# Kernel optimization log

Measured on AMD Instinct MI355X. Metric: run time of the kernel, lower is better.

Reference implementation:

```python
import jax, jax.numpy as jnp
import numpy as np

D_STATE = 64
HEADDIM = 64
D_CONV = 4
EPS = 1e-5


def _layernorm(x, w, b):
    m = jnp.mean(x, -1, keepdims=True)
    v = jnp.mean((x - m) ** 2, -1, keepdims=True)
    return (x - m) * jax.lax.rsqrt(v + EPS) * w + b


def _mamba2(x, W_in, conv_w, conv_b, dt_bias, A_log, Dh, rms_w, W_out):
    # Mamba2 (SSD) forward: in_proj -> causal depthwise conv + silu -> selective scan
    # -> gated RMSNorm -> out_proj.  ngroups=1, headdim=64, d_state=64.
    Bb, L, _ = x.shape
    d_inner = rms_w.shape[0]
    H = dt_bias.shape[0]
    P = d_inner // H
    conv_dim = d_inner + 2 * D_STATE
    zxbcdt = x @ W_in                                   # [B,L,2*d_inner+2*N+H]
    z = zxbcdt[..., :d_inner]
    xBC = zxbcdt[..., d_inner:d_inner + conv_dim]
    dt = zxbcdt[..., d_inner + conv_dim:]               # [B,L,H]
    # causal depthwise conv1d (kernel D_CONV) + bias + silu
    xpad = jnp.pad(xBC, ((0, 0), (D_CONV - 1, 0), (0, 0)))
    xBC = sum(conv_w[k] * xpad[:, k:k + L] for k in range(D_CONV)) + conv_b
    xBC = jax.nn.silu(xBC)
    xh = xBC[..., :d_inner].reshape(Bb, L, H, P)        # [B,L,H,P]
    Bm = xBC[..., d_inner:d_inner + D_STATE]            # [B,L,N]
    Cm = xBC[..., d_inner + D_STATE:]                   # [B,L,N]
    dt = jax.nn.softplus(dt + dt_bias)                  # [B,L,H]
    A = -jnp.exp(A_log)                                 # [H]
    da = jnp.exp(dt * A)                                # [B,L,H] discrete decay
    dtx = dt[..., None] * xh                            # [B,L,H,P]

    def step(h, inp):
        da_t, dtx_t, B_t, C_t = inp
        h = da_t[:, :, None, None] * h + jnp.einsum('bhp,bn->bhpn', dtx_t, B_t)
        y_t = jnp.einsum('bhpn,bn->bhp', h, C_t)
        return h, y_t

    h0 = jnp.zeros((Bb, H, P, D_STATE), x.dtype)
    _, y = jax.lax.scan(step, h0, (da.transpose(1, 0, 2), dtx.transpose(1, 0, 2, 3),
                                   Bm.transpose(1, 0, 2), Cm.transpose(1, 0, 2)))
    y = y.transpose(1, 0, 2, 3) + Dh[None, None, :, None] * xh   # skip term
    y = y.reshape(Bb, L, d_inner)
    # gated RMSNorm (norm_before_gate=False): rmsnorm(y * silu(z)) * weight
    y = y * jax.nn.silu(z)
    y = y * jax.lax.rsqrt(jnp.mean(y * y, -1, keepdims=True) + EPS) * rms_w
    return y @ W_out


def _mamba_params(key, d_model, pre):
    d_inner = 2 * d_model
    H = d_inner // HEADDIM
    conv_dim = d_inner + 2 * D_STATE
    d_in = 2 * d_inner + 2 * D_STATE + H
    k = jax.random.split(key, 5)
    return {
        pre + '_W_in': jax.random.normal(k[0], (d_model, d_in), jnp.float32) * (d_model ** -0.5),
        pre + '_conv_w': jax.random.normal(k[1], (D_CONV, conv_dim), jnp.float32) * 0.2,
        pre + '_conv_b': jnp.zeros((conv_dim,), jnp.float32),
        pre + '_dt_bias': jnp.log(jnp.expm1(jax.random.uniform(k[2], (H,), jnp.float32, 0.001, 0.1))),
        pre + '_A_log': jnp.log(jax.random.uniform(k[3], (H,), jnp.float32, 1.0, 16.0)),
        pre + '_D': jnp.ones((H,), jnp.float32),
        pre + '_rms_w': jnp.ones((d_inner,), jnp.float32),
        pre + '_W_out': jax.random.normal(k[4], (d_inner, d_model), jnp.float32) * (d_inner ** -0.5),
    }


def setup_inputs() -> dict:
    key = jax.random.key(0)
    ks = jax.random.split(key, 3)
    B, L, C = 8, 1024, 128
    inp = {'x': jax.random.normal(ks[0], (B, L, C), jnp.float32)}
    inp['ln_spa_w'] = jnp.ones((C,), jnp.float32)
    inp['ln_spa_b'] = jnp.zeros((C,), jnp.float32)
    inp['ln_spe_w'] = jnp.ones((L,), jnp.float32)
    inp['ln_spe_b'] = jnp.zeros((L,), jnp.float32)
    inp.update(_mamba_params(ks[1], C, 'spa'))
    inp.update(_mamba_params(ks[2], L, 'spe'))
    return inp


def reference(x, ln_spa_w, ln_spa_b, ln_spe_w, ln_spe_b,
              spa_W_in, spa_conv_w, spa_conv_b, spa_dt_bias, spa_A_log, spa_D, spa_rms_w, spa_W_out,
              spe_W_in, spe_conv_w, spe_conv_b, spe_dt_bias, spe_A_log, spe_D, spe_rms_w, spe_W_out):
    # SSD_Block.forward (drop_path=0 -> identity)
    x_spa = _layernorm(x, ln_spa_w, ln_spa_b)
    x_spa = _mamba2(x_spa, spa_W_in, spa_conv_w, spa_conv_b, spa_dt_bias,
                    spa_A_log, spa_D, spa_rms_w, spa_W_out) + x
    x_spe = x_spa.transpose(0, 2, 1)                      # [B,C,L]
    x_spe = _layernorm(x_spe, ln_spe_w, ln_spe_b)
    x_spe = _mamba2(x_spe, spe_W_in, spe_conv_w, spe_conv_b, spe_dt_bias,
                    spe_A_log, spe_D, spe_rms_w, spe_W_out)
    return x_spe.transpose(0, 2, 1) + x_spa
```

## Files before the change

kernel.cpp:

```cpp
#include <hip/hip_runtime.h>
#include <hip/hip_bf16.h>

#define EPSV 1e-5f

typedef __attribute__((ext_vector_type(8))) short short8v;
typedef __attribute__((ext_vector_type(4))) float f32x4;

__device__ inline unsigned short f2bf(float f) {
  __hip_bfloat16 h = __float2bfloat16(f);
  return *reinterpret_cast<unsigned short*>(&h);
}

__device__ inline float bf2f(unsigned short u) {
  return __uint_as_float(((unsigned int)u) << 16);
}

__device__ inline float siluf(float x) { return x / (1.f + expf(-x)); }

__device__ inline void gload_lds16(const void* g, void* l) {
  __builtin_amdgcn_global_load_lds(
      (const __attribute__((address_space(1))) void*)g,
      (__attribute__((address_space(3))) void*)l, 16, 0, 0);
}

__device__ inline float wave_prefix_incl(float v, int lane) {
  #pragma unroll
  for (int o = 1; o < 64; o <<= 1) {
    float u = __shfl_up(v, o);
    if (lane >= o) v += u;
  }
  return v;
}

__device__ inline void wtconv_tile(const float* __restrict__ W,
                                   unsigned short* __restrict__ Wt,
                                   int K, int N, int bx, int by) {
  __shared__ float tile[64][65];
  int n0 = bx * 64, k0 = by * 64;
  int tid = threadIdx.x;
  int r = tid >> 4, c4 = (tid & 15) * 4;
  #pragma unroll
  for (int i = 0; i < 4; i++) {
    int kk = r + i * 16;
    float4 v = make_float4(0.f, 0.f, 0.f, 0.f);
    if (n0 + c4 < N) v = *reinterpret_cast<const float4*>(&W[(long)(k0 + kk) * N + n0 + c4]);
    tile[kk][c4] = v.x; tile[kk][c4 + 1] = v.y; tile[kk][c4 + 2] = v.z; tile[kk][c4 + 3] = v.w;
  }
  __syncthreads();
  #pragma unroll
  for (int i = 0; i < 4; i++) {
    int nl = r + i * 16;
    if (n0 + nl < N) {
      ushort4 o;
      o.x = f2bf(tile[c4 + 0][nl]);
      o.y = f2bf(tile[c4 + 1][nl]);
      o.z = f2bf(tile[c4 + 2][nl]);
      o.w = f2bf(tile[c4 + 3][nl]);
      *reinterpret_cast<ushort4*>(&Wt[(long)(n0 + nl) * K + k0 + c4]) = o;
    }
  }
}

__global__ __launch_bounds__(256) void ln_wt_fused(const float* __restrict__ x,
                                                   const float* __restrict__ w,
                                                   const float* __restrict__ bb,
                                                   unsigned short* __restrict__ outA,
                                                   const float* __restrict__ W0,
                                                   unsigned short* __restrict__ T0,
                                                   const float* __restrict__ W1,
                                                   unsigned short* __restrict__ T1,
                                                   const float* __restrict__ W2,
                                                   unsigned short* __restrict__ T2,
                                                   const float* __restrict__ W3,
                                                   unsigned short* __restrict__ T3) {
  int id = blockIdx.x;
  if (id < 4096) {
    int tid = threadIdx.x;
    __shared__ float lds[4];
    long row = (long)id * 2 + (tid >> 7);
    int lane = tid & 127;
    int base = (tid >> 7) << 1;
    float v = x[row * 128 + lane];
    float s = v;
    #pragma unroll
    for (int o = 32; o; o >>= 1) s += __shfl_xor(s, o);
    if ((tid & 63) == 0) lds[tid >> 6] = s;
    __syncthreads();
    float m = (lds[base] + lds[base + 1]) * (1.f / 128.f);
    float d = v - m;
    float q = d * d;
    #pragma unroll
    for (int o = 32; o; o >>= 1) q += __shfl_xor(q, o);
    __syncthreads();
    if ((tid & 63) == 0) lds[tid >> 6] = q;
    __syncthreads();
    float inv = rsqrtf((lds[base] + lds[base + 1]) * (1.f / 128.f) + EPSV);
    outA[row * 128 + lane] = f2bf(d * inv * w[lane] + bb[lane]);
  } else {
    id -= 4096;
    if (id < 22)        { int r = id;        wtconv_tile(W0, T0, 128,  644,  r % 11, r / 11); }
    else if (id < 30)   { int r = id - 22;   wtconv_tile(W1, T1, 256,  128,  r % 2,  r / 2); }
    else if (id < 1102) { int r = id - 30;   wtconv_tile(W2, T2, 1024, 4256, r % 67, r / 67); }
    else                { int r = id - 1102; wtconv_tile(W3, T3, 2048, 1024, r % 16, r / 16); }
  }
}

__global__ __launch_bounds__(256) void spe_normT(const float* __restrict__ xspa,
                                                 const float* __restrict__ part2,
                                                 const float* __restrict__ w,
                                                 const float* __restrict__ bb,
                                                 unsigned short* __restrict__ out) {
  __shared__ float tile[128][65];
  int c0 = blockIdx.x * 64, l0 = blockIdx.y * 128, b = blockIdx.z;
  int tid = threadIdx.x;
  int rr = tid >> 4, c4 = (tid & 15) * 4;
  #pragma unroll
  for (int p = 0; p < 8; p++) {
    int l = rr + p * 16;
    f32x4 v = *reinterpret_cast<const f32x4*>(
        &xspa[((long)b * 1024 + l0 + l) * 128 + c0 + c4]);
    tile[l][c4] = v[0]; tile[l][c4 + 1] = v[1];
    tile[l][c4 + 2] = v[2]; tile[l][c4 + 3] = v[3];
  }
  __syncthreads();
  int ch = tid >> 2, lq = tid & 3;
  int gc = c0 + ch;
  int bx = gc >> 6, cl = gc & 63;
  float ssum = 0.f, qsum = 0.f;
  #pragma unroll
  for (int sub = 0; sub < 16; sub++) {
    int by = b * 16 + sub;
    float2 pq = *reinterpret_cast<const float2*>(&part2[(((by * 2 + bx) * 64) + cl) * 2]);
    ssum += pq.x; qsum += pq.y;
  }
  float mm = ssum * (1.f / 1024.f);
  float rstd = rsqrtf(qsum * (1.f / 1024.f) - mm * mm + EPSV);
  #pragma unroll
  for (int j = 0; j < 8; j++) {
    int qidx = lq + j * 4;
    int l = qidx * 4;
    float4 wv = *reinterpret_cast<const float4*>(&w[l0 + l]);
    float4 bv = *reinterpret_cast<const float4*>(&bb[l0 + l]);
    ushort4 o;
    o.x = f2bf((tile[l + 0][ch] - mm) * rstd * wv.x + bv.x);
    o.y = f2bf((tile[l + 1][ch] - mm) * rstd * wv.y + bv.y);
    o.z = f2bf((tile[l + 2][ch] - mm) * rstd * wv.z + bv.z);
    o.w = f2bf((tile[l + 3][ch] - mm) * rstd * wv.w + bv.w);
    *reinterpret_cast<ushort4*>(&out[((long)b * 128 + c0 + ch) * 1024 + l0 + l]) = o;
  }
}

__global__ __launch_bounds__(256) void gemm128_split(const unsigned short* __restrict__ A,
                                                     const unsigned short* __restrict__ Bt,
                                                     unsigned short* __restrict__ zout,
                                                     unsigned short* __restrict__ o2,
                                                     float* __restrict__ o3,
                                                     int M, int N, int K,
                                                     int c1, int c2) {
  __shared__ unsigned short As[2][128 * 32];
  __shared__ unsigned short Bs[2][128 * 32];
  int tid = threadIdx.x;
  int lane = tid & 63, w = tid >> 6;
  int wr = (w >> 1) * 64, wc = (w & 1) * 64;
  int ln15 = lane & 15, kg = lane >> 4;
  int rowBase = blockIdx.y * 128, colBase = blockIdx.x * 128;
  int srow = w * 32 + (lane >> 2);
  int scol = (lane & 3) * 8;
  f32x4 acc[4][4] = {};
  auto stage = [&](int buf, int k0) {
    gload_lds16(&A[(long)(rowBase + srow) * K + k0 + scol], &As[buf][(w * 32) * 32]);
    gload_lds16(&A[(long)(rowBase + srow + 16) * K + k0 + scol], &As[buf][(w * 32 + 16) * 32]);
    gload_lds16(&Bt[(long)(colBase + srow) * K + k0 + scol], &Bs[buf][(w * 32) * 32]);
    gload_lds16(&Bt[(long)(colBase + srow + 16) * K + k0 + scol], &Bs[buf][(w * 32 + 16) * 32]);
  };
  stage(0, 0);
  __syncthreads();
  int cur = 0;
  for (int k0 = 0; k0 < K; k0 += 32) {
    if (k0 + 32 < K) stage(cur ^ 1, k0 + 32);
    short8v af[4], bfr[4];
    #pragma unroll
    for (int mt = 0; mt < 4; mt++)
      af[mt] = *reinterpret_cast<const short8v*>(&As[cur][(wr + mt * 16 + ln15) * 32 + kg * 8]);
    #pragma unroll
    for (int nt = 0; nt < 4; nt++)
      bfr[nt] = *reinterpret_cast<const short8v*>(&Bs[cur][(wc + nt * 16 + ln15) * 32 + kg * 8]);
    #pragma unroll
    for (int mt = 0; mt < 4; mt++)
      #pragma unroll
      for (int nt = 0; nt < 4; nt++)
        acc[mt][nt] = __builtin_amdgcn_mfma_f32_16x16x32_bf16(af[mt], bfr[nt], acc[mt][nt], 0, 0, 0);
    __syncthreads();
    cur ^= 1;
  }
  #pragma unroll
  for (int mt = 0; mt < 4; mt++)
    #pragma unroll
    for (int nt = 0; nt < 4; nt++)
      #pragma unroll
      for (int q = 0; q < 4; q++) {
        int r = rowBase + wr + mt * 16 + kg * 4 + q;
        int c = colBase + wc + nt * 16 + ln15;
        if (c < N) {
          float v = acc[mt][nt][q];
          if (c < c1) zout[(long)r * c1 + c] = f2bf(v);
          else if (c < c2) o2[(long)r * (c2 - c1) + (c - c1)] = f2bf(v);
          else o3[(long)r * (N - c2) + (c - c2)] = v;
        }
      }
}

__global__ __launch_bounds__(256) void gemm128x64_t(const unsigned short* __restrict__ A,
                                                    const unsigned short* __restrict__ Bt,
                                                    const float* __restrict__ R,
                                                    float* __restrict__ out,
                                                    int M, int N, int K) {
  __shared__ unsigned short As[2][128 * 32];
  __shared__ unsigned short Bs[2][64 * 32];
  int tid = threadIdx.x;
  int lane = tid & 63, w = tid >> 6;
  int wr = w * 32;
  int ln15 = lane & 15, kg = lane >> 4;
  int rowBase = blockIdx.y * 128, colBase = blockIdx.x * 64;
  int arow = w * 32 + (lane >> 2);
  int brow = w * 16 + (lane >> 2);
  int scol = (lane & 3) * 8;
  f32x4 acc[2][4] = {};
  auto stage = [&](int buf, int k0) {
    gload_lds16(&A[(long)(rowBase + arow) * K + k0 + scol], &As[buf][(w * 32) * 32]);
    gload_lds16(&A[(long)(rowBase + arow + 16) * K + k0 + scol], &As[buf][(w * 32 + 16) * 32]);
    gload_lds16(&Bt[(long)(colBase + brow) * K + k0 + scol], &Bs[buf][(w * 16) * 32]);
  };
  stage(0, 0);
  __syncthreads();
  int cur = 0;
  for (int k0 = 0; k0 < K; k0 += 32) {
    if (k0 + 32 < K) stage(cur ^ 1, k0 + 32);
    short8v af[2], bfr[4];
    #pragma unroll
    for (int mt = 0; mt < 2; mt++)
      af[mt] = *reinterpret_cast<const short8v*>(&As[cur][(wr + mt * 16 + ln15) * 32 + kg * 8]);
    #pragma unroll
    for (int nt = 0; nt < 4; nt++)
      bfr[nt] = *reinterpret_cast<const short8v*>(&Bs[cur][(nt * 16 + ln15) * 32 + kg * 8]);
    #pragma unroll
    for (int mt = 0; mt < 2; mt++)
      #pragma unroll
      for (int nt = 0; nt < 4; nt++)
        acc[mt][nt] = __builtin_amdgcn_mfma_f32_16x16x32_bf16(af[mt], bfr[nt], acc[mt][nt], 0, 0, 0);
    __syncthreads();
    cur ^= 1;
  }
  #pragma unroll
  for (int mt = 0; mt < 2; mt++)
    #pragma unroll
    for (int nt = 0; nt < 4; nt++)
      #pragma unroll
      for (int q = 0; q < 4; q++) {
        int r = rowBase + wr + mt * 16 + kg * 4 + q;
        int c = colBase + nt * 16 + ln15;
        int bb = r >> 7, ch = r & 127;
        out[(long)bb * 131072 + (long)c * 128 + ch] =
            acc[mt][nt][q] + R[((long)bb * 1024 + c) * 128 + ch];
      }
}

__global__ __launch_bounds__(256) void gemm_mfma1(const unsigned short* __restrict__ A,
                                                  const unsigned short* __restrict__ Bt,
                                                  const float* __restrict__ R,
                                                  float* __restrict__ out,
                                                  float* __restrict__ part2,
                                                  int M, int N, int K) {
  __shared__ unsigned short As[2][64 * 32];
  __shared__ unsigned short Bs[2][64 * 32];
  int tid = threadIdx.x;
  int lane = tid & 63, w = tid >> 6;
  int wr = (w >> 1) * 32, wc = (w & 1) * 32;
  int ln15 = lane & 15, kg = lane >> 4;
  int rowBase = blockIdx.y * 64, colBase = blockIdx.x * 64;
  int srow = w * 16 + (lane >> 2);
  int scol = (lane & 3) * 8;
  f32x4 acc[2][2] = {};
  auto stage = [&](int buf, int k0) {
    gload_lds16(&A[(long)(rowBase + srow) * K + k0 + scol], &As[buf][(w * 16) * 32]);
    gload_lds16(&Bt[(long)(colBase + srow) * K + k0 + scol], &Bs[buf][(w * 16) * 32]);
  };
  stage(0, 0);
  __syncthreads();
  int cur = 0;
  for (int k0 = 0; k0 < K; k0 += 32) {
    if (k0 + 32 < K) stage(cur ^ 1, k0 + 32);
    short8v af[2], bfr[2];
    #pragma unroll
    for (int mt = 0; mt < 2; mt++)
      af[mt] = *reinterpret_cast<const short8v*>(&As[cur][(wr + mt * 16 + ln15) * 32 + kg * 8]);
    #pragma unroll
    for (int nt = 0; nt < 2; nt++)
      bfr[nt] = *reinterpret_cast<const short8v*>(&Bs[cur][(wc + nt * 16 + ln15) * 32 + kg * 8]);
    #pragma unroll
    for (int mt = 0; mt < 2; mt++)
      #pragma unroll
      for (int nt = 0; nt < 2; nt++)
        acc[mt][nt] = __builtin_amdgcn_mfma_f32_16x16x32_bf16(af[mt], bfr[nt], acc[mt][nt], 0, 0, 0);
    __syncthreads();
    cur ^= 1;
  }
  float sC[2] = {0.f, 0.f}, qC[2] = {0.f, 0.f};
  #pragma unroll
  for (int mt = 0; mt < 2; mt++)
    #pragma unroll
    for (int nt = 0; nt < 2; nt++)
      #pragma unroll
      for (int q = 0; q < 4; q++) {
        int r = rowBase + wr + mt * 16 + kg * 4 + q;
        int c = colBase + wc + nt * 16 + ln15;
        float v = acc[mt][nt][q] + R[(long)r * N + c];
        out[(long)r * N + c] = v;
        sC[nt] += v;
        qC[nt] += v * v;
      }
  __shared__ float redS[4][32], redQ[4][32];
  #pragma unroll
  for (int nt = 0; nt < 2; nt++) {
    sC[nt] += __shfl_xor(sC[nt], 16);
    sC[nt] += __shfl_xor(sC[nt], 32);
    qC[nt] += __shfl_xor(qC[nt], 16);
    qC[nt] += __shfl_xor(qC[nt], 32);
  }
  if (lane < 16) {
    redS[w][ln15] = sC[0];       redQ[w][ln15] = qC[0];
    redS[w][16 + ln15] = sC[1];  redQ[w][16 + ln15] = qC[1];
  }
  __syncthreads();
  if (tid < 64) {
    int c = tid;
    int grp = c >> 5, lo = c & 31;
    float ss = redS[grp][lo] + redS[grp + 2][lo];
    float qq = redQ[grp][lo] + redQ[grp + 2][lo];
    long slot = ((long)(blockIdx.y * 2 + blockIdx.x) * 64 + c) * 2;
    part2[slot] = ss;
    part2[slot + 1] = qq;
  }
}

__global__ __launch_bounds__(256) void conv_dtda(const unsigned short* __restrict__ zx,
                                                 const float* __restrict__ cw,
                                                 const float* __restrict__ cb,
                                                 unsigned short* __restrict__ cout,
                                                 const float* __restrict__ raw,
                                                 const float* __restrict__ dtbias,
                                                 const float* __restrict__ alog,
                                                 float* __restrict__ dt,
                                                 float* __restrict__ la,
                                                 int Bb, int L, int conv_dim,
                                                 int H, int rowsH, int convBlocks) {
  int tid = threadIdx.x;
  if ((int)blockIdx.x < convBlocks) {
    long idx4 = (long)blockIdx.x * 256 + tid;
    int nch4 = conv_dim >> 2;
    long total4 = (long)Bb * L * nch4;
    if (idx4 >= total4) return;
    int ch = (int)(idx4 % nch4) << 2;
    long rt = idx4 / nch4;
    int t = (int)(rt % L);
    int b = (int)(rt / L);
    f32x4 acc = *reinterpret_cast<const f32x4*>(&cb[ch]);
    #pragma unroll
    for (int k = 0; k < 4; k++) {
      int tt = t + k - 3;
      if (tt >= 0) {
        f32x4 wv = *reinterpret_cast<const f32x4*>(&cw[k * conv_dim + ch]);
        ushort4 zu = *reinterpret_cast<const ushort4*>(
            &zx[((long)b * L + tt) * conv_dim + ch]);
        acc[0] += wv[0] * bf2f(zu.x);
        acc[1] += wv[1] * bf2f(zu.y);
        acc[2] += wv[2] * bf2f(zu.z);
        acc[3] += wv[3] * bf2f(zu.w);
      }
    }
    ushort4 o;
    o.x = f2bf(siluf(acc[0])); o.y = f2bf(siluf(acc[1]));
    o.z = f2bf(siluf(acc[2])); o.w = f2bf(siluf(acc[3]));
    *reinterpret_cast<ushort4*>(&cout[rt * conv_dim + ch]) = o;
  } else {
    int idx = ((int)blockIdx.x - convBlocks) * 256 + tid;
    if (idx >= rowsH) return;
    int h = idx % H;
    float v = raw[idx] + dtbias[h];
    float sp = (v > 20.f) ? v : log1pf(expf(v));
    dt[idx] = sp;
    la[idx] = -expf(alog[h]) * sp;
  }
}

__global__ __launch_bounds__(256) void ssd_local(const unsigned short* __restrict__ xbc,
                                                 const float* __restrict__ dtv,
                                                 const float* __restrict__ la,
                                                 float* __restrict__ Sc,
                                                 float* __restrict__ Aprod,
                                                 int NC, int nc_launch, int H,
                                                 int conv_dim, int d_inner) {
  int blk = blockIdx.x;
  int c = blk % nc_launch, bh = blk / nc_launch;
  int h = bh % H, b = bh / H;
  int tid = threadIdx.x;
  long row0 = ((long)(b * NC + c)) * 64;
  __shared__ unsigned short XpT[64 * 72];
  __shared__ unsigned short BT[64 * 72];
  __shared__ float Ws[64];
  int tq = tid >> 4, cq = (tid & 15) << 2;
  ushort4 xr[4], br[4];
  #pragma unroll
  for (int i = 0; i < 4; i++) {
    int t = tq + i * 16;
    const unsigned short* rp = xbc + (row0 + t) * conv_dim;
    xr[i] = *reinterpret_cast<const ushort4*>(rp + (h << 6) + cq);
    br[i] = *reinterpret_cast<const ushort4*>(rp + d_inner + cq);
  }
  if (tid < 64) {
    long r = (row0 + tid) * H + h;
    float cum = wave_prefix_incl(la[r], tid);
    float cT = __shfl(cum, 63);
    Ws[tid] = expf(cT - cum) * dtv[r];
    if (tid == 63) Aprod[(long)bh * NC + c] = expf(cT);
  }
  __syncthreads();
  #pragma unroll
  for (int i = 0; i < 4; i++) {
    int t = tq + i * 16;
    float wv = Ws[t];
    XpT[(cq + 0) * 72 + t] = f2bf(wv * bf2f(xr[i].x));
    XpT[(cq + 1) * 72 + t] = f2bf(wv * bf2f(xr[i].y));
    XpT[(cq + 2) * 72 + t] = f2bf(wv * bf2f(xr[i].z));
    XpT[(cq + 3) * 72 + t] = f2bf(wv * bf2f(xr[i].w));
    BT[(cq + 0) * 72 + t] = br[i].x;
    BT[(cq + 1) * 72 + t] = br[i].y;
    BT[(cq + 2) * 72 + t] = br[i].z;
    BT[(cq + 3) * 72 + t] = br[i].w;
  }
  __syncthreads();
  int lane = tid & 63, wv2 = tid >> 6;
  int wr = (wv2 >> 1) * 32, wc = (wv2 & 1) * 32;
  int ln15 = lane & 15, kg = lane >> 4;
  f32x4 acc[2][2] = {};
  #pragma unroll
  for (int ks = 0; ks < 2; ks++) {
    short8v af[2], bq[2];
    #pragma unroll
    for (int mt = 0; mt < 2; mt++)
      af[mt] = *reinterpret_cast<const short8v*>(&XpT[(wr + mt * 16 + ln15) * 72 + ks * 32 + kg * 8]);
    #pragma unroll
    for (int nt = 0; nt < 2; nt++)
      bq[nt] = *reinterpret_cast<const short8v*>(&BT[(wc + nt * 16 + ln15) * 72 + ks * 32 + kg * 8]);
    #pragma unroll
    for (int mt = 0; mt < 2; mt++)
      #pragma unroll
      for (int nt = 0; nt < 2; nt++)
        acc[mt][nt] = __builtin_amdgcn_mfma_f32_16x16x32_bf16(af[mt], bq[nt], acc[mt][nt], 0, 0, 0);
  }
  float* base = Sc + ((long)bh * NC + c) * 4096;
  #pragma unroll
  for (int mt = 0; mt < 2; mt++)
    #pragma unroll
    for (int nt = 0; nt < 2; nt++)
      #pragma unroll
      for (int q = 0; q < 4; q++) {
        int p = wr + mt * 16 + kg * 4 + q;
        int n = wc + nt * 16 + ln15;
        base[p * 64 + n] = acc[mt][nt][q];
      }
}

__global__ __launch_bounds__(256) void ssd_out(const unsigned short* __restrict__ xbc,
                                               const float* __restrict__ dtv,
                                               const float* __restrict__ la,
                                               const float* __restrict__ Sc,
                                               const float* __restrict__ Aprod,
                                               const float* __restrict__ Dvec,
                                               unsigned short* __restrict__ y,
                                               int NC, int H, int conv_dim,
                                               int d_inner) {
  int blk = blockIdx.x;
  int c = blk % NC, bh = blk / NC;
  int h = bh % H, b = bh / H;
  int tid = threadIdx.x;
  long row0 = ((long)(b * NC + c)) * 64;
  __shared__ unsigned short Cb[64 * 72];
  __shared__ unsigned short Bb[64 * 72];
  __shared__ unsigned short XT[64 * 72];
  __shared__ unsigned short hb[64 * 72];
  __shared__ float Cum[64], Dt[64];
  int tq = tid >> 4, cq = (tid & 15) << 2;
  #pragma unroll
  for (int i = 0; i < 4; i++) {
    int t = tq + i * 16;
    const unsigned short* rp = xbc + (row0 + t) * conv_dim;
    ushort4 cu = *reinterpret_cast<const ushort4*>(rp + d_inner + 64 + cq);
    ushort4 bu = *reinterpret_cast<const ushort4*>(rp + d_inner + cq);
    ushort4 xu = *reinterpret_cast<const ushort4*>(rp + (h << 6) + cq);
    *reinterpret_cast<ushort4*>(&Cb[t * 72 + cq]) = cu;
    *reinterpret_cast<ushort4*>(&Bb[t * 72 + cq]) = bu;
    XT[(cq + 0) * 72 + t] = xu.x;
    XT[(cq + 1) * 72 + t] = xu.y;
    XT[(cq + 2) * 72 + t] = xu.z;
    XT[(cq + 3) * 72 + t] = xu.w;
  }
  if (c > 0) {
    f32x4 hreg[4] = {};
    const float* ap = Aprod + (long)bh * NC;
    for (int j = 0; j < c; j++) {
      const float* sb = Sc + ((long)bh * NC + j) * 4096;
      float a = ap[j];
      #pragma unroll
      for (int i = 0; i < 4; i++) {
        int p = tq + i * 16;
        f32x4 sv = *reinterpret_cast<const f32x4*>(&sb[p * 64 + cq]);
        hreg[i] = hreg[i] * a + sv;
      }
    }
    #pragma unroll
    for (int i = 0; i < 4; i++) {
      int p = tq + i * 16;
      ushort4 ho;
      ho.x = f2bf(hreg[i][0]); ho.y = f2bf(hreg[i][1]);
      ho.z = f2bf(hreg[i][2]); ho.w = f2bf(hreg[i][3]);
      *reinterpret_cast<ushort4*>(&hb[p * 72 + cq]) = ho;
    }
  }
  if (tid < 64) {
    long r = (row0 + tid) * H + h;
    Cum[tid] = wave_prefix_incl(la[r], tid);
    Dt[tid] = dtv[r];
  }
  __syncthreads();
  int lane = tid & 63, wv2 = tid >> 6;
  int wr = (wv2 >> 1) * 32, wc = (wv2 & 1) * 32;
  int ln15 = lane & 15, kg = lane >> 4;
  f32x4 accA[2][2] = {};
  #pragma unroll
  for (int ks = 0; ks < 2; ks++) {
    short8v af[2], bq[2];
    #pragma unroll
    for (int mt = 0; mt < 2; mt++)
      af[mt] = *reinterpret_cast<const short8v*>(&Cb[(wr + mt * 16 + ln15) * 72 + ks * 32 + kg * 8]);
    #pragma unroll
    for (int nt = 0; nt < 2; nt++)
      bq[nt] = *reinterpret_cast<const short8v*>(&Bb[(wc + nt * 16 + ln15) * 72 + ks * 32 + kg * 8]);
    #pragma unroll
    for (int mt = 0; mt < 2; mt++)
      #pragma unroll
      for (int nt = 0; nt < 2; nt++)
        accA[mt][nt] = __builtin_amdgcn_mfma_f32_16x16x32_bf16(af[mt], bq[nt], accA[mt][nt], 0, 0, 0);
  }
  unsigned short gmb[2][2][4];
  #pragma unroll
  for (int mt = 0; mt < 2; mt++)
    #pragma unroll
    for (int nt = 0; nt < 2; nt++)
      #pragma unroll
      for (int q = 0; q < 4; q++) {
        int t = wr + mt * 16 + kg * 4 + q;
        int s = wc + nt * 16 + ln15;
        float v = (s <= t) ? accA[mt][nt][q] * expf(Cum[t] - Cum[s]) * Dt[s] : 0.f;
        gmb[mt][nt][q] = f2bf(v);
      }
  __syncthreads();
  #pragma unroll
  for (int mt = 0; mt < 2; mt++)
    #pragma unroll
    for (int nt = 0; nt < 2; nt++)
      #pragma unroll
      for (int q = 0; q < 4; q++)
        Bb[(wr + mt * 16 + kg * 4 + q) * 72 + wc + nt * 16 + ln15] = gmb[mt][nt][q];
  __syncthreads();
  f32x4 accY[2][2] = {}, accZ[2][2] = {};
  #pragma unroll
  for (int ks = 0; ks < 2; ks++) {
    short8v af[2], bq[2];
    #pragma unroll
    for (int mt = 0; mt < 2; mt++)
      af[mt] = *reinterpret_cast<const short8v*>(&Bb[(wr + mt * 16 + ln15) * 72 + ks * 32 + kg * 8]);
    #pragma unroll
    for (int nt = 0; nt < 2; nt++)
      bq[nt] = *reinterpret_cast<const short8v*>(&XT[(wc + nt * 16 + ln15) * 72 + ks * 32 + kg * 8]);
    #pragma unroll
    for (int mt = 0; mt < 2; mt++)
      #pragma unroll
      for (int nt = 0; nt < 2; nt++)
        accY[mt][nt] = __builtin_amdgcn_mfma_f32_16x16x32_bf16(af[mt], bq[nt], accY[mt][nt], 0, 0, 0);
  }
  if (c > 0) {
    #pragma unroll
    for (int ks = 0; ks < 2; ks++) {
      short8v af[2], bq[2];
      #pragma unroll
      for (int mt = 0; mt < 2; mt++)
        af[mt] = *reinterpret_cast<const short8v*>(&Cb[(wr + mt * 16 + ln15) * 72 + ks * 32 + kg * 8]);
      #pragma unroll
      for (int nt = 0; nt < 2; nt++)
        bq[nt] = *reinterpret_cast<const short8v*>(&hb[(wc + nt * 16 + ln15) * 72 + ks * 32 + kg * 8]);
      #pragma unroll
      for (int mt = 0; mt < 2; mt++)
        #pragma unroll
        for (int nt = 0; nt < 2; nt++)
          accZ[mt][nt] = __builtin_amdgcn_mfma_f32_16x16x32_bf16(af[mt], bq[nt], accZ[mt][nt], 0, 0, 0);
    }
  }
  float Dv = Dvec[h];
  #pragma unroll
  for (int mt = 0; mt < 2; mt++)
    #pragma unroll
    for (int q = 0; q < 4; q++) {
      int t = wr + mt * 16 + kg * 4 + q;
      float wB = expf(Cum[t]);
      const unsigned short* xp = xbc + (row0 + t) * conv_dim + (h << 6);
      unsigned short* yp = y + (row0 + t) * d_inner + (h << 6);
      #pragma unroll
      for (int nt = 0; nt < 2; nt++) {
        int p = wc + nt * 16 + ln15;
        yp[p] = f2bf(accY[mt][nt][q] + accZ[mt][nt][q] * wB + bf2f(xp[p]) * Dv);
      }
    }
}

__global__ __launch_bounds__(256) void ssd_spe2(const unsigned short* __restrict__ xbc,
                                                const float* __restrict__ dtv,
                                                const float* __restrict__ la,
                                                const float* __restrict__ Dvec,
                                                unsigned short* __restrict__ y,
                                                int H, int conv_dim, int d_inner) {
  int bh = blockIdx.x;
  int h = bh % H, b = bh / H;
  int tid = threadIdx.x;
  __shared__ unsigned short Cb[64 * 72];
  __shared__ unsigned short Bb[64 * 72];
  __shared__ unsigned short XT[64 * 72];
  __shared__ unsigned short BT2[64 * 72];
  __shared__ unsigned short WXT[64 * 72];
  __shared__ unsigned short hb[64 * 72];
  __shared__ float Cum[64], Dt[64], Wsh[64];
  int tq = tid >> 4, cq = (tid & 15) << 2;
  int lane = tid & 63, wv2 = tid >> 6;
  int wr = (wv2 >> 1) * 32, wc = (wv2 & 1) * 32;
  int ln15 = lane & 15, kg = lane >> 4;
  float Dv = Dvec[h];

  long row0 = (long)b * 128;
  ushort4 cu[4], bu[4], xu[4];
  #pragma unroll
  for (int i = 0; i < 4; i++) {
    int t = tq + i * 16;
    const unsigned short* rp = xbc + (row0 + t) * conv_dim;
    cu[i] = *reinterpret_cast<const ushort4*>(rp + d_inner + 64 + cq);
    bu[i] = *reinterpret_cast<const ushort4*>(rp + d_inner + cq);
    xu[i] = *reinterpret_cast<const ushort4*>(rp + (h << 6) + cq);
  }
  if (tid < 64) {
    long r = (row0 + tid) * H + h;
    float cum = wave_prefix_incl(la[r], tid);
    float cT = __shfl(cum, 63);
    Cum[tid] = cum;
    Dt[tid] = dtv[r];
    Wsh[tid] = expf(cT - cum) * dtv[r];
  }
  __syncthreads();
  #pragma unroll
  for (int i = 0; i < 4; i++) {
    int t = tq + i * 16;
    float wvv = Wsh[t];
    *reinterpret_cast<ushort4*>(&Cb[t * 72 + cq]) = cu[i];
    *reinterpret_cast<ushort4*>(&Bb[t * 72 + cq]) = bu[i];
    XT[(cq + 0) * 72 + t] = xu[i].x;
    XT[(cq + 1) * 72 + t] = xu[i].y;
    XT[(cq + 2) * 72 + t] = xu[i].z;
    XT[(cq + 3) * 72 + t] = xu[i].w;
    BT2[(cq + 0) * 72 + t] = bu[i].x;
    BT2[(cq + 1) * 72 + t] = bu[i].y;
    BT2[(cq + 2) * 72 + t] = bu[i].z;
    BT2[(cq + 3) * 72 + t] = bu[i].w;
    WXT[(cq + 0) * 72 + t] = f2bf(wvv * bf2f(xu[i].x));
    WXT[(cq + 1) * 72 + t] = f2bf(wvv * bf2f(xu[i].y));
    WXT[(cq + 2) * 72 + t] = f2bf(wvv * bf2f(xu[i].z));
    WXT[(cq + 3) * 72 + t] = f2bf(wvv * bf2f(xu[i].w));
  }
  __syncthreads();
  f32x4 accS[2][2] = {};
  #pragma unroll
  for (int ks = 0; ks < 2; ks++) {
    short8v af[2], bq[2];
    #pragma unroll
    for (int mt = 0; mt < 2; mt++)
      af[mt] = *reinterpret_cast<const short8v*>(&WXT[(wr + mt * 16 + ln15) * 72 + ks * 32 + kg * 8]);
    #pragma unroll
    for (int nt = 0; nt < 2; nt++)
      bq[nt] = *reinterpret_cast<const short8v*>(&BT2[(wc + nt * 16 + ln15) * 72 + ks * 32 + kg * 8]);
    #pragma unroll
    for (int mt = 0; mt < 2; mt++)
      #pragma unroll
      for (int nt = 0; nt < 2; nt++)
        accS[mt][nt] = __builtin_amdgcn_mfma_f32_16x16x32_bf16(af[mt], bq[nt], accS[mt][nt], 0, 0, 0);
  }
  f32x4 accA[2][2] = {};
  #pragma unroll
  for (int ks = 0; ks < 2; ks++) {
    short8v af[2], bq[2];
    #pragma unroll
    for (int mt = 0; mt < 2; mt++)
      af[mt] = *reinterpret_cast<const short8v*>(&Cb[(wr + mt * 16 + ln15) * 72 + ks * 32 + kg * 8]);
    #pragma unroll
    for (int nt = 0; nt < 2; nt++)
      bq[nt] = *reinterpret_cast<const short8v*>(&Bb[(wc + nt * 16 + ln15) * 72 + ks * 32 + kg * 8]);
    #pragma unroll
    for (int mt = 0; mt < 2; mt++)
      #pragma unroll
      for (int nt = 0; nt < 2; nt++)
        accA[mt][nt] = __builtin_amdgcn_mfma_f32_16x16x32_bf16(af[mt], bq[nt], accA[mt][nt], 0, 0, 0);
  }
  unsigned short gmb[2][2][4];
  #pragma unroll
  for (int mt = 0; mt < 2; mt++)
    #pragma unroll
    for (int nt = 0; nt < 2; nt++)
      #pragma unroll
      for (int q = 0; q < 4; q++) {
        int t = wr + mt * 16 + kg * 4 + q;
        int s = wc + nt * 16 + ln15;
        float v = (s <= t) ? accA[mt][nt][q] * expf(Cum[t] - Cum[s]) * Dt[s] : 0.f;
        gmb[mt][nt][q] = f2bf(v);
      }
  __syncthreads();
  #pragma unroll
  for (int mt = 0; mt < 2; mt++)
    #pragma unroll
    for (int nt = 0; nt < 2; nt++)
      #pragma unroll
      for (int q = 0; q < 4; q++) {
        Bb[(wr + mt * 16 + kg * 4 + q) * 72 + wc + nt * 16 + ln15] = gmb[mt][nt][q];
        int p = wr + mt * 16 + kg * 4 + q;
        int n = wc + nt * 16 + ln15;
        hb[p * 72 + n] = f2bf(accS[mt][nt][q]);
      }
  __syncthreads();
  f32x4 accY[2][2] = {};
  #pragma unroll
  for (int ks = 0; ks < 2; ks++) {
    short8v af[2], bq[2];
    #pragma unroll
    for (int mt = 0; mt < 2; mt++)
      af[mt] = *reinterpret_cast<const short8v*>(&Bb[(wr + mt * 16 + ln15) * 72 + ks * 32 + kg * 8]);
    #pragma unroll
    for (int nt = 0; nt < 2; nt++)
      bq[nt] = *reinterpret_cast<const short8v*>(&XT[(wc + nt * 16 + ln15) * 72 + ks * 32 + kg * 8]);
    #pragma unroll
    for (int mt = 0; mt < 2; mt++)
      #pragma unroll
      for (int nt = 0; nt < 2; nt++)
        accY[mt][nt] = __builtin_amdgcn_mfma_f32_16x16x32_bf16(af[mt], bq[nt], accY[mt][nt], 0, 0, 0);
  }
  #pragma unroll
  for (int mt = 0; mt < 2; mt++)
    #pragma unroll
    for (int q = 0; q < 4; q++) {
      int t = wr + mt * 16 + kg * 4 + q;
      const unsigned short* xp = xbc + (row0 + t) * conv_dim + (h << 6);
      unsigned short* yp = y + (row0 + t) * d_inner + (h << 6);
      #pragma unroll
      for (int nt = 0; nt < 2; nt++) {
        int p = wc + nt * 16 + ln15;
        yp[p] = f2bf(accY[mt][nt][q] + bf2f(xp[p]) * Dv);
      }
    }
  __syncthreads();

  long row1 = row0 + 64;
  #pragma unroll
  for (int i = 0; i < 4; i++) {
    int t = tq + i * 16;
    const unsigned short* rp = xbc + (row1 + t) * conv_dim;
    cu[i] = *reinterpret_cast<const ushort4*>(rp + d_inner + 64 + cq);
    bu[i] = *reinterpret_cast<const ushort4*>(rp + d_inner + cq);
    xu[i] = *reinterpret_cast<const ushort4*>(rp + (h << 6) + cq);
  }
  if (tid < 64) {
    long r = (row1 + tid) * H + h;
    Cum[tid] = wave_prefix_incl(la[r], tid);
    Dt[tid] = dtv[r];
  }
  __syncthreads();
  #pragma unroll
  for (int i = 0; i < 4; i++) {
    int t = tq + i * 16;
    *reinterpret_cast<ushort4*>(&Cb[t * 72 + cq]) = cu[i];
    *reinterpret_cast<ushort4*>(&Bb[t * 72 + cq]) = bu[i];
    XT[(cq + 0) * 72 + t] = xu[i].x;
    XT[(cq + 1) * 72 + t] = xu[i].y;
    XT[(cq + 2) * 72 + t] = xu[i].z;
    XT[(cq + 3) * 72 + t] = xu[i].w;
  }
  __syncthreads();
  f32x4 accA1[2][2] = {};
  #pragma unroll
  for (int ks = 0; ks < 2; ks++) {
    short8v af[2], bq[2];
    #pragma unroll
    for (int mt = 0; mt < 2; mt++)
      af[mt] = *reinterpret_cast<const short8v*>(&Cb[(wr + mt * 16 + ln15) * 72 + ks * 32 + kg * 8]);
    #pragma unroll
    for (int nt = 0; nt < 2; nt++)
      bq[nt] = *reinterpret_cast<const short8v*>(&Bb[(wc + nt * 16 + ln15) * 72 + ks * 32 + kg * 8]);
    #pragma unroll
    for (int mt = 0; mt < 2; mt++)
      #pragma unroll
      for (int nt = 0; nt < 2; nt++)
        accA1[mt][nt] = __builtin_amdgcn_mfma_f32_16x16x32_bf16(af[mt], bq[nt], accA1[mt][nt], 0, 0, 0);
  }
  #pragma unroll
  for (int mt = 0; mt < 2; mt++)
    #pragma unroll
    for (int nt = 0; nt < 2; nt++)
      #pragma unroll
      for (int q = 0; q < 4; q++) {
        int t = wr + mt * 16 + kg * 4 + q;
        int s = wc + nt * 16 + ln15;
        float v = (s <= t) ? accA1[mt][nt][q] * expf(Cum[t] - Cum[s]) * Dt[s] : 0.f;
        gmb[mt][nt][q] = f2bf(v);
      }
  __syncthreads();
  #pragma unroll
  for (int mt = 0; mt < 2; mt++)
    #pragma unroll
    for (int nt = 0; nt < 2; nt++)
      #pragma unroll
      for (int q = 0; q < 4; q++)
        Bb[(wr + mt * 16 + kg * 4 + q) * 72 + wc + nt * 16 + ln15] = gmb[mt][nt][q];
  __syncthreads();
  f32x4 accY1[2][2] = {}, accZ1[2][2] = {};
  #pragma unroll
  for (int ks = 0; ks < 2; ks++) {
    short8v af[2], bq[2];
    #pragma unroll
    for (int mt = 0; mt < 2; mt++)
      af[mt] = *reinterpret_cast<const short8v*>(&Bb[(wr + mt * 16 + ln15) * 72 + ks * 32 + kg * 8]);
    #pragma unroll
    for (int nt = 0; nt < 2; nt++)
      bq[nt] = *reinterpret_cast<const short8v*>(&XT[(wc + nt * 16 + ln15) * 72 + ks * 32 + kg * 8]);
    #pragma unroll
    for (int mt = 0; mt < 2; mt++)
      #pragma unroll
      for (int nt = 0; nt < 2; nt++)
        accY1[mt][nt] = __builtin_amdgcn_mfma_f32_16x16x32_bf16(af[mt], bq[nt], accY1[mt][nt], 0, 0, 0);
  }
  #pragma unroll
  for (int ks = 0; ks < 2; ks++) {
    short8v af[2], bq[2];
    #pragma unroll
    for (int mt = 0; mt < 2; mt++)
      af[mt] = *reinterpret_cast<const short8v*>(&Cb[(wr + mt * 16 + ln15) * 72 + ks * 32 + kg * 8]);
    #pragma unroll
    for (int nt = 0; nt < 2; nt++)
      bq[nt] = *reinterpret_cast<const short8v*>(&hb[(wc + nt * 16 + ln15) * 72 + ks * 32 + kg * 8]);
    #pragma unroll
    for (int mt = 0; mt < 2; mt++)
      #pragma unroll
      for (int nt = 0; nt < 2; nt++)
        accZ1[mt][nt] = __builtin_amdgcn_mfma_f32_16x16x32_bf16(af[mt], bq[nt], accZ1[mt][nt], 0, 0, 0);
  }
  #pragma unroll
  for (int mt = 0; mt < 2; mt++)
    #pragma unroll
    for (int q = 0; q < 4; q++) {
      int t = wr + mt * 16 + kg * 4 + q;
      float wB = expf(Cum[t]);
      const unsigned short* xp = xbc + (row1 + t) * conv_dim + (h << 6);
      unsigned short* yp = y + (row1 + t) * d_inner + (h << 6);
      #pragma unroll
      for (int nt = 0; nt < 2; nt++) {
        int p = wc + nt * 16 + ln15;
        yp[p] = f2bf(accY1[mt][nt][q] + accZ1[mt][nt][q] * wB + bf2f(xp[p]) * Dv);
      }
    }
}

template <int CPL>
__global__ __launch_bounds__(256) void gate_rms_bf16(const unsigned short* __restrict__ y,
                                                     const unsigned short* __restrict__ z,
                                                     const float* __restrict__ rmsw,
                                                     unsigned short* __restrict__ ab,
                                                     int d_inner) {
  long row = (long)blockIdx.x * 4 + (threadIdx.x >> 6);
  int lane = threadIdx.x & 63;
  const unsigned short* yr = y + row * d_inner;
  const unsigned short* zr = z + row * d_inner;
  float g[CPL];
  float ss = 0.f;
  #pragma unroll
  for (int j = 0; j < CPL / 4; j++) {
    int c = j * 256 + lane * 4;
    ushort4 yv = *reinterpret_cast<const ushort4*>(&yr[c]);
    ushort4 zv = *reinterpret_cast<const ushort4*>(&zr[c]);
    float g0 = bf2f(yv.x) * siluf(bf2f(zv.x));
    float g1 = bf2f(yv.y) * siluf(bf2f(zv.y));
    float g2 = bf2f(yv.z) * siluf(bf2f(zv.z));
    float g3 = bf2f(yv.w) * siluf(bf2f(zv.w));
    g[j * 4 + 0] = g0; g[j * 4 + 1] = g1; g[j * 4 + 2] = g2; g[j * 4 + 3] = g3;
    ss += g0 * g0 + g1 * g1 + g2 * g2 + g3 * g3;
  }
  #pragma unroll
  for (int o = 32; o; o >>= 1) ss += __shfl_xor(ss, o);
  float inv = rsqrtf(ss / (float)d_inner + EPSV);
  #pragma unroll
  for (int j = 0; j < CPL / 4; j++) {
    int c = j * 256 + lane * 4;
    float4 wv = *reinterpret_cast<const float4*>(&rmsw[c]);
    ushort4 o;
    o.x = f2bf(g[j * 4 + 0] * inv * wv.x);
    o.y = f2bf(g[j * 4 + 1] * inv * wv.y);
    o.z = f2bf(g[j * 4 + 2] * inv * wv.z);
    o.w = f2bf(g[j * 4 + 3] * inv * wv.w);
    *reinterpret_cast<ushort4*>(&ab[row * d_inner + c]) = o;
  }
}

extern "C" void kernel_launch(void* const* d_in, const int* in_sizes, int n_in,
                              void* d_out, int out_size, void* d_ws,
                              size_t ws_size, hipStream_t stream) {
  const float* x        = (const float*)d_in[0];
  const float* ln_spa_w = (const float*)d_in[1];
  const float* ln_spa_b = (const float*)d_in[2];
  const float* ln_spe_w = (const float*)d_in[3];
  const float* ln_spe_b = (const float*)d_in[4];
  const float* spa_W_in   = (const float*)d_in[5];
  const float* spa_conv_w = (const float*)d_in[6];
  const float* spa_conv_b = (const float*)d_in[7];
  const float* spa_dt_b   = (const float*)d_in[8];
  const float* spa_A_log  = (const float*)d_in[9];
  const float* spa_D      = (const float*)d_in[10];
  const float* spa_rms_w  = (const float*)d_in[11];
  const float* spa_W_out  = (const float*)d_in[12];
  const float* spe_W_in   = (const float*)d_in[13];
  const float* spe_conv_w = (const float*)d_in[14];
  const float* spe_conv_b = (const float*)d_in[15];
  const float* spe_dt_b   = (const float*)d_in[16];
  const float* spe_A_log  = (const float*)d_in[17];
  const float* spe_D      = (const float*)d_in[18];
  const float* spe_rms_w  = (const float*)d_in[19];
  const float* spe_W_out  = (const float*)d_in[20];
  float* out = (float*)d_out;

  float* ws = (float*)d_ws;
  float* xspa   = ws;
  unsigned short* z = (unsigned short*)(ws + 1048576);
  unsigned short* xbcraw = (unsigned short*)(ws + 3145728);
  float* Sc     = ws + 3145728;
  float* dtraw  = ws + 6291456;
  unsigned short* cv = (unsigned short*)(ws + 6324224);
  float* dtb    = ws + 9469952;
  float* la     = ws + 9502720;
  unsigned short* yb = (unsigned short*)(ws + 9535488);
  unsigned short* Abf     = (unsigned short*)(ws + 11634688);
  unsigned short* Wt_spai = (unsigned short*)(ws + 12683264);
  unsigned short* Wt_spao = (unsigned short*)(ws + 12724480);
  unsigned short* Wt_spei = (unsigned short*)(ws + 12740864);
  unsigned short* Wt_speo = (unsigned short*)(ws + 14919936);

  hipLaunchKernelGGL(ln_wt_fused, dim3(5710), dim3(256), 0, stream,
                     x, ln_spa_w, ln_spa_b, Abf,
                     spa_W_in, Wt_spai, spa_W_out, Wt_spao,
                     spe_W_in, Wt_spei, spe_W_out, Wt_speo);

  hipLaunchKernelGGL(gemm128_split, dim3(6, 64), dim3(256), 0, stream,
                     Abf, Wt_spai, z, xbcraw, dtraw,
                     8192, 644, 128, 256, 640);
  hipLaunchKernelGGL(conv_dtda, dim3(3200), dim3(256), 0, stream,
                     xbcraw, spa_conv_w, spa_conv_b, cv,
                     dtraw, spa_dt_b, spa_A_log, dtb, la,
                     8, 1024, 384, 4, 32768, 3072);
  hipLaunchKernelGGL(ssd_local, dim3(480), dim3(256), 0, stream,
                     cv, dtb, la, Sc, dtraw, 16, 15, 4, 384, 256);
  hipLaunchKernelGGL(ssd_out, dim3(512), dim3(256), 0, stream,
                     cv, dtb, la, Sc, dtraw, spa_D, yb, 16, 4, 384, 256);
  hipLaunchKernelGGL((gate_rms_bf16<4>), dim3(2048), dim3(256), 0, stream,
                     yb, z, spa_rms_w, Abf, 256);
  hipLaunchKernelGGL(gemm_mfma1, dim3(2, 128), dim3(256), 0, stream,
                     Abf, Wt_spao, x, xspa, dtb, 8192, 128, 256);

  hipLaunchKernelGGL(spe_normT, dim3(2, 8, 8), dim3(256), 0, stream,
                     xspa, dtb, ln_spe_w, ln_spe_b, Abf);
  hipLaunchKernelGGL(gemm128_split, dim3(34, 8), dim3(256), 0, stream,
                     Abf, Wt_spei, z, xbcraw, dtraw,
                     1024, 4256, 1024, 2048, 4224);
  hipLaunchKernelGGL(conv_dtda, dim3(2304), dim3(256), 0, stream,
                     xbcraw, spe_conv_w, spe_conv_b, cv,
                     dtraw, spe_dt_b, spe_A_log, dtb, la,
                     8, 128, 2176, 32, 32768, 2176);
  hipLaunchKernelGGL(ssd_spe2, dim3(256), dim3(256), 0, stream,
                     cv, dtb, la, spe_D, yb, 32, 2176, 2048);
  hipLaunchKernelGGL((gate_rms_bf16<32>), dim3(256), dim3(256), 0, stream,
                     yb, z, spe_rms_w, Abf, 2048);
  hipLaunchKernelGGL(gemm128x64_t, dim3(16, 8), dim3(256), 0, stream,
                     Abf, Wt_speo, xspa, out, 1024, 1024, 2048);
}
```

Baseline: 157.9 us.

## Spread weight transpose-convert tiles across later kernels to overlap with compute

The first kernel no longer converts all four weight matrices to transposed bf16. Only the spatial input-projection weights are converted there. The spatial out-proj and spectral in-proj tiles are appended as extra blocks to the spatial conv_dtda launch, and the spectral out-proj tiles are appended to the ssd_local launch. This shortens the critical path of the first kernel and lets the weight conversion fill idle CUs in later, smaller launches. Each weight is still converted before its consumer GEMM runs. The cost is extra blocks in those kernels that may compete with their main work.

```diff
diff --git a/kernel.cpp b/kernel.cpp
--- a/kernel.cpp
+++ b/kernel.cpp
@@ -61,18 +61,12 @@
   }
 }
 
-__global__ __launch_bounds__(256) void ln_wt_fused(const float* __restrict__ x,
-                                                   const float* __restrict__ w,
-                                                   const float* __restrict__ bb,
-                                                   unsigned short* __restrict__ outA,
-                                                   const float* __restrict__ W0,
-                                                   unsigned short* __restrict__ T0,
-                                                   const float* __restrict__ W1,
-                                                   unsigned short* __restrict__ T1,
-                                                   const float* __restrict__ W2,
-                                                   unsigned short* __restrict__ T2,
-                                                   const float* __restrict__ W3,
-                                                   unsigned short* __restrict__ T3) {
+__global__ __launch_bounds__(256) void ln_wt0(const float* __restrict__ x,
+                                              const float* __restrict__ w,
+                                              const float* __restrict__ bb,
+                                              unsigned short* __restrict__ outA,
+                                              const float* __restrict__ W0,
+                                              unsigned short* __restrict__ T0) {
   int id = blockIdx.x;
   if (id < 4096) {
     int tid = threadIdx.x;
@@ -97,11 +91,8 @@
     float inv = rsqrtf((lds[base] + lds[base + 1]) * (1.f / 128.f) + EPSV);
     outA[row * 128 + lane] = f2bf(d * inv * w[lane] + bb[lane]);
   } else {
-    id -= 4096;
-    if (id < 22)        { int r = id;        wtconv_tile(W0, T0, 128,  644,  r % 11, r / 11); }
-    else if (id < 30)   { int r = id - 22;   wtconv_tile(W1, T1, 256,  128,  r % 2,  r / 2); }
-    else if (id < 1102) { int r = id - 30;   wtconv_tile(W2, T2, 1024, 4256, r % 67, r / 67); }
-    else                { int r = id - 1102; wtconv_tile(W3, T3, 2048, 1024, r % 16, r / 16); }
+    int r = id - 4096;
+    wtconv_tile(W0, T0, 128, 644, r % 11, r / 11);
   }
 }
 
@@ -353,10 +344,22 @@
                                                  float* __restrict__ dt,
                                                  float* __restrict__ la,
                                                  int Bb, int L, int conv_dim,
-                                                 int H, int rowsH, int convBlocks) {
+                                                 int H, int rowsH, int convBlocks,
+                                                 const float* __restrict__ Wa,
+                                                 unsigned short* __restrict__ Ta,
+                                                 const float* __restrict__ Wb,
+                                                 unsigned short* __restrict__ Tb,
+                                                 int wtBase) {
+  int bid = blockIdx.x;
   int tid = threadIdx.x;
-  if ((int)blockIdx.x < convBlocks) {
-    long idx4 = (long)blockIdx.x * 256 + tid;
+  if (bid >= wtBase) {
+    int id = bid - wtBase;
+    if (id < 8) wtconv_tile(Wa, Ta, 256, 128, id % 2, id / 2);
+    else { int r = id - 8; wtconv_tile(Wb, Tb, 1024, 4256, r % 67, r / 67); }
+    return;
+  }
+  if (bid < convBlocks) {
+    long idx4 = (long)bid * 256 + tid;
     int nch4 = conv_dim >> 2;
     long total4 = (long)Bb * L * nch4;
     if (idx4 >= total4) return;
@@ -383,7 +386,7 @@
     o.z = f2bf(siluf(acc[2])); o.w = f2bf(siluf(acc[3]));
     *reinterpret_cast<ushort4*>(&cout[rt * conv_dim + ch]) = o;
   } else {
-    int idx = ((int)blockIdx.x - convBlocks) * 256 + tid;
+    int idx = (bid - convBlocks) * 256 + tid;
     if (idx >= rowsH) return;
     int h = idx % H;
     float v = raw[idx] + dtbias[h];
@@ -399,8 +402,16 @@
                                                  float* __restrict__ Sc,
                                                  float* __restrict__ Aprod,
                                                  int NC, int nc_launch, int H,
-                                                 int conv_dim, int d_inner) {
+                                                 int conv_dim, int d_inner,
+                                                 const float* __restrict__ Wc,
+                                                 unsigned short* __restrict__ Tc,
+                                                 int wtBase) {
   int blk = blockIdx.x;
+  if (blk >= wtBase) {
+    int r = blk - wtBase;
+    wtconv_tile(Wc, Tc, 2048, 1024, r % 16, r / 16);
+    return;
+  }
   int c = blk % nc_launch, bh = blk / nc_launch;
   int h = bh % H, b = bh / H;
   int tid = threadIdx.x;
@@ -963,20 +974,20 @@
   unsigned short* Wt_spei = (unsigned short*)(ws + 12740864);
   unsigned short* Wt_speo = (unsigned short*)(ws + 14919936);
 
-  hipLaunchKernelGGL(ln_wt_fused, dim3(5710), dim3(256), 0, stream,
-                     x, ln_spa_w, ln_spa_b, Abf,
-                     spa_W_in, Wt_spai, spa_W_out, Wt_spao,
-                     spe_W_in, Wt_spei, spe_W_out, Wt_speo);
+  hipLaunchKernelGGL(ln_wt0, dim3(4118), dim3(256), 0, stream,
+                     x, ln_spa_w, ln_spa_b, Abf, spa_W_in, Wt_spai);
 
   hipLaunchKernelGGL(gemm128_split, dim3(6, 64), dim3(256), 0, stream,
                      Abf, Wt_spai, z, xbcraw, dtraw,
                      8192, 644, 128, 256, 640);
-  hipLaunchKernelGGL(conv_dtda, dim3(3200), dim3(256), 0, stream,
+  hipLaunchKernelGGL(conv_dtda, dim3(4280), dim3(256), 0, stream,
                      xbcraw, spa_conv_w, spa_conv_b, cv,
                      dtraw, spa_dt_b, spa_A_log, dtb, la,
-                     8, 1024, 384, 4, 32768, 3072);
-  hipLaunchKernelGGL(ssd_local, dim3(480), dim3(256), 0, stream,
-                     cv, dtb, la, Sc, dtraw, 16, 15, 4, 384, 256);
+                     8, 1024, 384, 4, 32768, 3072,
+                     spa_W_out, Wt_spao, spe_W_in, Wt_spei, 3200);
+  hipLaunchKernelGGL(ssd_local, dim3(992), dim3(256), 0, stream,
+                     cv, dtb, la, Sc, dtraw, 16, 15, 4, 384, 256,
+                     spe_W_out, Wt_speo, 480);
   hipLaunchKernelGGL(ssd_out, dim3(512), dim3(256), 0, stream,
                      cv, dtb, la, Sc, dtraw, spa_D, yb, 16, 4, 384, 256);
   hipLaunchKernelGGL((gate_rms_bf16<4>), dim3(2048), dim3(256), 0, stream,
@@ -992,7 +1003,8 @@
   hipLaunchKernelGGL(conv_dtda, dim3(2304), dim3(256), 0, stream,
                      xbcraw, spe_conv_w, spe_conv_b, cv,
                      dtraw, spe_dt_b, spe_A_log, dtb, la,
-                     8, 128, 2176, 32, 32768, 2176);
+                     8, 128, 2176, 32, 32768, 2176,
+                     spa_W_out, Wt_spao, spe_W_in, Wt_spei, 2304);
   hipLaunchKernelGGL(ssd_spe2, dim3(256), dim3(256), 0, stream,
                      cv, dtb, la, spe_D, yb, 32, 2176, 2048);
   hipLaunchKernelGGL((gate_rms_bf16<32>), dim3(256), dim3(256), 0, stream,
```

New measurement: 157.1 us. About the same (-0.5%).
